# Performance work log

Hardware: AMD Instinct MI355X
Metric: run time of the kernel (lower is better)

The kernel has to match this reference:

```python
import jax, jax.numpy as jnp
import numpy as np

EPS = 1e-6
TEMP = 1.0
L = 64  # shapelet_len


def _znorm(a):
    # z-normalize over last axis, population std, clamped by EPS (matches torch unbiased=False + clamp_min)
    mean = a.mean(axis=-1, keepdims=True)
    std = jnp.maximum(a.std(axis=-1, keepdims=True), EPS)
    return (a - mean) / std


def setup_inputs() -> dict:
    key = jax.random.key(0)
    k1, k2 = jax.random.split(key)
    bs, T, C, P = 32, 8192, 1, 64
    x = jax.random.normal(k1, (bs, T, C), dtype=jnp.float32)
    shapelets = jax.random.normal(k2, (P, C, L), dtype=jnp.float32)
    return {"x": x, "shapelets": shapelets}


def reference(x, shapelets):
    # x: [bs, T, C]; shapelets: [P, C, L]
    bs, T, C = x.shape
    P = shapelets.shape[0]
    x_ct = jnp.transpose(x, (0, 2, 1))  # [bs, C, T]
    Tp = T - L + 1
    # sliding windows: [bs, C, T', L]
    idx = jnp.arange(Tp)[:, None] + jnp.arange(L)[None, :]
    w = x_ct[:, :, idx]
    # z-normalize windows and shapelets over the length axis
    w = _znorm(w)
    s = _znorm(shapelets)
    # squared euclidean distance via expansion ||w||^2 - 2 w.s + ||s||^2 (sum over C and L)
    w2 = jnp.sum(w * w, axis=(1, 3))          # [bs, T']
    s2 = jnp.sum(s * s, axis=(1, 2))          # [P]
    dot = jnp.einsum('bctl,pcl->btp', w, s)   # [bs, T', P]
    dist2 = w2[:, :, None] + s2[None, None, :] - 2.0 * dot
    temp = max(TEMP, EPS)
    act = jnp.exp(-dist2 / temp)              # [bs, T', P]
    # center-pad to length T: left = L//2, right = T - (T' + left)
    left = L // 2
    right = max(0, T - (Tp + left))
    act_full = jnp.pad(act, ((0, 0), (left, right), (0, 0)))
    return act_full[:, :T, :]
```

## Files before the change

### kernel.cpp

```cpp
#include <hip/hip_runtime.h>
#include <math.h>

#define T_LEN 8192
#define EPSF  1e-6f

typedef __attribute__((ext_vector_type(8))) short short8;
typedef __attribute__((ext_vector_type(4))) float float4v;

__global__ __launch_bounds__(256, 4) void shapelet_fused(
        const float* __restrict__ x,
        const float* __restrict__ sh,
        float* __restrict__ out) {
    __shared__ float Sraw[64][65];
    __shared__ unsigned short Bhi[64][72];
    __shared__ unsigned short Blo[64][72];
    __shared__ float xs[320];
    __shared__ float lmu[256], linv[256], lw2[256];
    __shared__ __align__(16) float lsum[64];
    __shared__ __align__(16) float ls2[64];

    const int tid  = threadIdx.x;
    const int lane = tid & 63;
    const int wave = tid >> 6;
    const int n    = lane & 15;
    const int quad = lane >> 4;

    const int super = blockIdx.x & 31;
    const int b     = blockIdx.x >> 5;
    const int t0    = super << 8;

    {
        const float4* g4 = (const float4*)sh;
#pragma unroll
        for (int i = 0; i < 4; ++i) {
            int idx = tid + (i << 8);
            float4 v = g4[idx];
            int e = idx << 2;
            int row = e >> 6, col = e & 63;
            Sraw[row][col + 0] = v.x;
            Sraw[row][col + 1] = v.y;
            Sraw[row][col + 2] = v.z;
            Sraw[row][col + 3] = v.w;
        }
        if (tid < 80) {
            int g0 = t0 - 32 + (tid << 2);
            float4 v;
            if (g0 >= 0 && g0 + 3 < T_LEN) {
                v = *(const float4*)(x + (size_t)b * T_LEN + g0);
            } else {
                float* vp = (float*)&v;
#pragma unroll
                for (int e = 0; e < 4; ++e) {
                    int g = g0 + e;
                    vp[e] = ((unsigned)g < (unsigned)T_LEN) ? x[(size_t)b * T_LEN + g] : 0.f;
                }
            }
            *(float4*)&xs[tid << 2] = v;
        }
    }
    __syncthreads();

    if (tid < 64) {
        const int p = tid;
        const int c = ((p & 3) << 4) + (p >> 2);
        float s1 = 0.f;
        for (int l = 0; l < 64; ++l) s1 += Sraw[p][l];
        float mu = s1 * (1.f / 64.f);
        float sq = 0.f;
        for (int l = 0; l < 64; ++l) { float d = Sraw[p][l] - mu; sq = fmaf(d, d, sq); }
        float sd  = fmaxf(sqrtf(sq * (1.f / 64.f)), EPSF);
        float inv = 1.f / sd;
        float ssum = 0.f, ss2 = 0.f;
        for (int l2 = 0; l2 < 32; ++l2) {
            unsigned pk_h, pk_l;
            {
                float v = Sraw[p][2 * l2];
                float s = (v - mu) * inv;
                unsigned ub = __float_as_uint(s);
                float hi = __uint_as_float(ub & 0xFFFF0000u);
                float lo = s - hi;
                unsigned lb = __float_as_uint(lo) & 0xFFFF0000u;
                pk_h = ub >> 16;
                pk_l = lb >> 16;
                float eff = hi + __uint_as_float(lb);
                ssum += eff;
                ss2  = fmaf(eff, eff, ss2);
            }
            {
                float v = Sraw[p][2 * l2 + 1];
                float s = (v - mu) * inv;
                unsigned ub = __float_as_uint(s);
                float hi = __uint_as_float(ub & 0xFFFF0000u);
                float lo = s - hi;
                unsigned lb = __float_as_uint(lo) & 0xFFFF0000u;
                pk_h |= (ub & 0xFFFF0000u);
                pk_l |= lb;
                float eff = hi + __uint_as_float(lb);
                ssum += eff;
                ss2  = fmaf(eff, eff, ss2);
            }
            *(unsigned*)&Bhi[c][2 * l2] = pk_h;
            *(unsigned*)&Blo[c][2 * l2] = pk_l;
        }
        lsum[p] = ssum;
        ls2[p]  = ss2;
    } else {
        int r = tid - 64;
#pragma unroll
        for (int pass = 0; pass < 2; ++pass) {
            if (pass == 0 || r < 64 + 192) {
                float s1 = 0.f, sq = 0.f;
#pragma unroll
                for (int l = 0; l < 64; ++l) {
                    float v = xs[r + l];
                    s1 += v; sq = fmaf(v, v, sq);
                }
                float mu  = s1 * (1.f / 64.f);
                float var = fmaxf(sq * (1.f / 64.f) - mu * mu, 0.f);
                float sd  = fmaxf(sqrtf(var), EPSF);
                float inv = 1.f / sd;
                lmu[r]  = mu;
                linv[r] = inv;
                lw2[r]  = 64.f * var * inv * inv;
            }
            if (tid >= 128) break;
            r = tid - 64 + 192;
            if (pass == 1) break;
        }
    }
    __syncthreads();

    short8 Bh[4][2], Bl[4][2];
#pragma unroll
    for (int pt = 0; pt < 4; ++pt)
#pragma unroll
        for (int h = 0; h < 2; ++h) {
            Bh[pt][h] = *(const short8*)&Bhi[pt * 16 + n][h * 32 + (quad << 3)];
            Bl[pt][h] = *(const short8*)&Blo[pt * 16 + n][h * 32 + (quad << 3)];
        }
    const float4 sm4 = *(const float4*)&lsum[n << 2];
    const float4 sv4 = *(const float4*)&ls2[n << 2];

#pragma unroll
    for (int u = 0; u < 4; ++u) {
        const int abase = (u << 6) + (wave << 4) + n + (quad << 3);
        short8 Ah[2], Al[2];
#pragma unroll
        for (int h = 0; h < 2; ++h) {
#pragma unroll
            for (int j = 0; j < 8; ++j) {
                float v = xs[abase + h * 32 + j];
                unsigned ub = __float_as_uint(v);
                unsigned hb = ub & 0xFFFF0000u;
                float lo = v - __uint_as_float(hb);
                Ah[h][j] = (short)(ub >> 16);
                Al[h][j] = (short)(__float_as_uint(lo) >> 16);
            }
        }

        float4v acc[4];
#pragma unroll
        for (int pt = 0; pt < 4; ++pt) {
            float4v a = {0.f, 0.f, 0.f, 0.f};
#pragma unroll
            for (int h = 0; h < 2; ++h) {
                a = __builtin_amdgcn_mfma_f32_16x16x32_bf16(Ah[h], Bh[pt][h], a, 0, 0, 0);
                a = __builtin_amdgcn_mfma_f32_16x16x32_bf16(Ah[h], Bl[pt][h], a, 0, 0, 0);
                a = __builtin_amdgcn_mfma_f32_16x16x32_bf16(Al[h], Bh[pt][h], a, 0, 0, 0);
            }
            acc[pt] = a;
        }

#pragma unroll
        for (int r = 0; r < 4; ++r) {
            int tl = (u << 6) + (wave << 4) + (quad << 2) + r;
            int tg = t0 + tl;
            bool valid = (tg >= 32) && (tg <= 8160);
            float mu  = lmu[tl];
            float inv = linv[tl];
            float w2  = lw2[tl];
            float d0 = (acc[0][r] - mu * sm4.x) * inv;
            float d1 = (acc[1][r] - mu * sm4.y) * inv;
            float d2 = (acc[2][r] - mu * sm4.z) * inv;
            float d3 = (acc[3][r] - mu * sm4.w) * inv;
            float4 o;
            o.x = valid ? __expf(-(w2 + sv4.x - 2.f * d0)) : 0.f;
            o.y = valid ? __expf(-(w2 + sv4.y - 2.f * d1)) : 0.f;
            o.z = valid ? __expf(-(w2 + sv4.z - 2.f * d2)) : 0.f;
            o.w = valid ? __expf(-(w2 + sv4.w - 2.f * d3)) : 0.f;
            *(float4*)(out + (((size_t)(b * T_LEN + tg)) << 6) + (n << 2)) = o;
        }
    }
}

extern "C" void kernel_launch(void* const* d_in, const int* in_sizes, int n_in,
                              void* d_out, int out_size, void* d_ws, size_t ws_size,
                              hipStream_t stream) {
    const float* x  = (const float*)d_in[0];
    const float* sh = (const float*)d_in[1];
    float* out = (float*)d_out;

    shapelet_fused<<<32 * 32, 256, 0, stream>>>(x, sh, out);
}
```

Baseline: 82.94 us.

## Split shapelet normalization into a one-block prep kernel and read it from workspace

Moves the per-block shapelet z-normalization and bf16 hi/lo packing into a separate single-block kernel that writes packed operands and norms to the workspace, so the 1024 main blocks no longer redo it. The main kernel loads its MFMA B fragments directly from global memory, which removes the large shared arrays and one serial phase. It also packs the window statistics into one float4 per row, so each row needs a single shared read. The cost is an extra kernel launch and serialization before the main kernel.

```diff
diff --git a/kernel.cpp b/kernel.cpp
--- a/kernel.cpp
+++ b/kernel.cpp
@@ -7,17 +7,80 @@
 typedef __attribute__((ext_vector_type(8))) short short8;
 typedef __attribute__((ext_vector_type(4))) float float4v;
 
-__global__ __launch_bounds__(256, 4) void shapelet_fused(
+
+__global__ __launch_bounds__(64, 1) void shapelet_prep(
+        const float* __restrict__ sh, void* __restrict__ ws) {
+    unsigned short* Bhi_g = (unsigned short*)ws;
+    unsigned short* Blo_g = Bhi_g + 64 * 64;
+    float* lsum_g = (float*)((char*)ws + 16384);
+    float* ls2_g  = lsum_g + 64;
+
+    const int p = threadIdx.x;
+    const int c = ((p & 3) << 4) + (p >> 2);
+
+    float S[64];
+    const float4* s4 = (const float4*)(sh + (size_t)p * 64);
+#pragma unroll
+    for (int i = 0; i < 16; ++i) {
+        float4 v = s4[i];
+        S[4 * i + 0] = v.x;
+        S[4 * i + 1] = v.y;
+        S[4 * i + 2] = v.z;
+        S[4 * i + 3] = v.w;
+    }
+
+    float s1 = 0.f;
+#pragma unroll
+    for (int l = 0; l < 64; ++l) s1 += S[l];
+    float mu = s1 * (1.f / 64.f);
+    float sq = 0.f;
+#pragma unroll
+    for (int l = 0; l < 64; ++l) { float d = S[l] - mu; sq = fmaf(d, d, sq); }
+    float sd  = fmaxf(sqrtf(sq * (1.f / 64.f)), EPSF);
+    float inv = 1.f / sd;
+    float ssum = 0.f, ss2 = 0.f;
+#pragma unroll
+    for (int l2 = 0; l2 < 32; ++l2) {
+        unsigned pk_h, pk_l;
+        {
+            float v = S[2 * l2];
+            float s = (v - mu) * inv;
+            unsigned ub = __float_as_uint(s);
+            float hi = __uint_as_float(ub & 0xFFFF0000u);
+            float lo = s - hi;
+            unsigned lb = __float_as_uint(lo) & 0xFFFF0000u;
+            pk_h = ub >> 16;
+            pk_l = lb >> 16;
+            float eff = hi + __uint_as_float(lb);
+            ssum += eff;
+            ss2  = fmaf(eff, eff, ss2);
+        }
+        {
+            float v = S[2 * l2 + 1];
+            float s = (v - mu) * inv;
+            unsigned ub = __float_as_uint(s);
+            float hi = __uint_as_float(ub & 0xFFFF0000u);
+            float lo = s - hi;
+            unsigned lb = __float_as_uint(lo) & 0xFFFF0000u;
+            pk_h |= (ub & 0xFFFF0000u);
+            pk_l |= lb;
+            float eff = hi + __uint_as_float(lb);
+            ssum += eff;
+            ss2  = fmaf(eff, eff, ss2);
+        }
+        *(unsigned*)&Bhi_g[c * 64 + 2 * l2] = pk_h;
+        *(unsigned*)&Blo_g[c * 64 + 2 * l2] = pk_l;
+    }
+    lsum_g[p] = ssum;
+    ls2_g[p]  = ss2;
+}
+
+__global__ __launch_bounds__(256, 4) void shapelet_main(
         const float* __restrict__ x,
-        const float* __restrict__ sh,
+        const void* __restrict__ ws,
         float* __restrict__ out) {
-    __shared__ float Sraw[64][65];
-    __shared__ unsigned short Bhi[64][72];
-    __shared__ unsigned short Blo[64][72];
-    __shared__ float xs[320];
-    __shared__ float lmu[256], linv[256], lw2[256];
-    __shared__ __align__(16) float lsum[64];
-    __shared__ __align__(16) float ls2[64];
+    __shared__ __align__(16) float xs[320];
+    __shared__ float4 lstat[256];
 
     const int tid  = threadIdx.x;
     const int lane = tid & 63;
@@ -29,117 +92,59 @@
     const int b     = blockIdx.x >> 5;
     const int t0    = super << 8;
 
+    const unsigned short* Bhi_g = (const unsigned short*)ws;
+    const unsigned short* Blo_g = Bhi_g + 64 * 64;
+    const float* lsum_g = (const float*)((const char*)ws + 16384);
+
+    short8 Bh[4][2], Bl[4][2];
+#pragma unroll
+    for (int pt = 0; pt < 4; ++pt)
+#pragma unroll
+        for (int h = 0; h < 2; ++h) {
+            int off = ((pt * 16 + n) << 6) + (h << 5) + (quad << 3);
+            Bh[pt][h] = *(const short8*)(Bhi_g + off);
+            Bl[pt][h] = *(const short8*)(Blo_g + off);
+        }
+    const float4 sm4 = *(const float4*)(lsum_g + (n << 2));
+    const float4 sv4 = *(const float4*)(lsum_g + 64 + (n << 2));
+
+    if (tid < 80) {
+        int g0 = t0 - 32 + (tid << 2);
+        float4 v;
+        if (g0 >= 0 && g0 + 3 < T_LEN) {
+            v = *(const float4*)(x + (size_t)b * T_LEN + g0);
+        } else {
+            float* vp = (float*)&v;
+#pragma unroll
+            for (int e = 0; e < 4; ++e) {
+                int g = g0 + e;
+                vp[e] = ((unsigned)g < (unsigned)T_LEN) ? x[(size_t)b * T_LEN + g] : 0.f;
+            }
+        }
+        *(float4*)&xs[tid << 2] = v;
+    }
+    __syncthreads();
+
     {
-        const float4* g4 = (const float4*)sh;
-#pragma unroll
-        for (int i = 0; i < 4; ++i) {
-            int idx = tid + (i << 8);
-            float4 v = g4[idx];
-            int e = idx << 2;
-            int row = e >> 6, col = e & 63;
-            Sraw[row][col + 0] = v.x;
-            Sraw[row][col + 1] = v.y;
-            Sraw[row][col + 2] = v.z;
-            Sraw[row][col + 3] = v.w;
-        }
-        if (tid < 80) {
-            int g0 = t0 - 32 + (tid << 2);
-            float4 v;
-            if (g0 >= 0 && g0 + 3 < T_LEN) {
-                v = *(const float4*)(x + (size_t)b * T_LEN + g0);
-            } else {
-                float* vp = (float*)&v;
-#pragma unroll
-                for (int e = 0; e < 4; ++e) {
-                    int g = g0 + e;
-                    vp[e] = ((unsigned)g < (unsigned)T_LEN) ? x[(size_t)b * T_LEN + g] : 0.f;
-                }
-            }
-            *(float4*)&xs[tid << 2] = v;
-        }
+        const int r = tid;
+        float s1 = 0.f, sq = 0.f;
+#pragma unroll
+        for (int l = 0; l < 64; ++l) {
+            float v = xs[r + l];
+            s1 += v; sq = fmaf(v, v, sq);
+        }
+        float mu  = s1 * (1.f / 64.f);
+        float var = fmaxf(sq * (1.f / 64.f) - mu * mu, 0.f);
+        float sd  = fmaxf(sqrtf(var), EPSF);
+        float inv = 1.f / sd;
+        float4 st;
+        st.x = mu;
+        st.y = inv;
+        st.z = 64.f * var * inv * inv;
+        st.w = 0.f;
+        lstat[r] = st;
     }
     __syncthreads();
-
-    if (tid < 64) {
-        const int p = tid;
-        const int c = ((p & 3) << 4) + (p >> 2);
-        float s1 = 0.f;
-        for (int l = 0; l < 64; ++l) s1 += Sraw[p][l];
-        float mu = s1 * (1.f / 64.f);
-        float sq = 0.f;
-        for (int l = 0; l < 64; ++l) { float d = Sraw[p][l] - mu; sq = fmaf(d, d, sq); }
-        float sd  = fmaxf(sqrtf(sq * (1.f / 64.f)), EPSF);
-        float inv = 1.f / sd;
-        float ssum = 0.f, ss2 = 0.f;
-        for (int l2 = 0; l2 < 32; ++l2) {
-            unsigned pk_h, pk_l;
-            {
-                float v = Sraw[p][2 * l2];
-                float s = (v - mu) * inv;
-                unsigned ub = __float_as_uint(s);
-                float hi = __uint_as_float(ub & 0xFFFF0000u);
-                float lo = s - hi;
-                unsigned lb = __float_as_uint(lo) & 0xFFFF0000u;
-                pk_h = ub >> 16;
-                pk_l = lb >> 16;
-                float eff = hi + __uint_as_float(lb);
-                ssum += eff;
-                ss2  = fmaf(eff, eff, ss2);
-            }
-            {
-                float v = Sraw[p][2 * l2 + 1];
-                float s = (v - mu) * inv;
-                unsigned ub = __float_as_uint(s);
-                float hi = __uint_as_float(ub & 0xFFFF0000u);
-                float lo = s - hi;
-                unsigned lb = __float_as_uint(lo) & 0xFFFF0000u;
-                pk_h |= (ub & 0xFFFF0000u);
-                pk_l |= lb;
-                float eff = hi + __uint_as_float(lb);
-                ssum += eff;
-                ss2  = fmaf(eff, eff, ss2);
-            }
-            *(unsigned*)&Bhi[c][2 * l2] = pk_h;
-            *(unsigned*)&Blo[c][2 * l2] = pk_l;
-        }
-        lsum[p] = ssum;
-        ls2[p]  = ss2;
-    } else {
-        int r = tid - 64;
-#pragma unroll
-        for (int pass = 0; pass < 2; ++pass) {
-            if (pass == 0 || r < 64 + 192) {
-                float s1 = 0.f, sq = 0.f;
-#pragma unroll
-                for (int l = 0; l < 64; ++l) {
-                    float v = xs[r + l];
-                    s1 += v; sq = fmaf(v, v, sq);
-                }
-                float mu  = s1 * (1.f / 64.f);
-                float var = fmaxf(sq * (1.f / 64.f) - mu * mu, 0.f);
-                float sd  = fmaxf(sqrtf(var), EPSF);
-                float inv = 1.f / sd;
-                lmu[r]  = mu;
-                linv[r] = inv;
-                lw2[r]  = 64.f * var * inv * inv;
-            }
-            if (tid >= 128) break;
-            r = tid - 64 + 192;
-            if (pass == 1) break;
-        }
-    }
-    __syncthreads();
-
-    short8 Bh[4][2], Bl[4][2];
-#pragma unroll
-    for (int pt = 0; pt < 4; ++pt)
-#pragma unroll
-        for (int h = 0; h < 2; ++h) {
-            Bh[pt][h] = *(const short8*)&Bhi[pt * 16 + n][h * 32 + (quad << 3)];
-            Bl[pt][h] = *(const short8*)&Blo[pt * 16 + n][h * 32 + (quad << 3)];
-        }
-    const float4 sm4 = *(const float4*)&lsum[n << 2];
-    const float4 sv4 = *(const float4*)&ls2[n << 2];
 
 #pragma unroll
     for (int u = 0; u < 4; ++u) {
@@ -176,9 +181,10 @@
             int tl = (u << 6) + (wave << 4) + (quad << 2) + r;
             int tg = t0 + tl;
             bool valid = (tg >= 32) && (tg <= 8160);
-            float mu  = lmu[tl];
-            float inv = linv[tl];
-            float w2  = lw2[tl];
+            float4 st = lstat[tl];
+            float mu  = st.x;
+            float inv = st.y;
+            float w2  = st.z;
             float d0 = (acc[0][r] - mu * sm4.x) * inv;
             float d1 = (acc[1][r] - mu * sm4.y) * inv;
             float d2 = (acc[2][r] - mu * sm4.z) * inv;
@@ -200,5 +206,6 @@
     const float* sh = (const float*)d_in[1];
     float* out = (float*)d_out;
 
-    shapelet_fused<<<32 * 32, 256, 0, stream>>>(x, sh, out);
+    shapelet_prep<<<1, 64, 0, stream>>>(sh, d_ws);
+    shapelet_main<<<32 * 32, 256, 0, stream>>>(x, d_ws, out);
 }
```

After: 87.24 us. +5.2%, slower.
